# Kernel optimization log

Measured on AMD Instinct MI355X. Metric: run time of the kernel, lower is better.

The kernel has to match this reference:

```python
import jax, jax.numpy as jnp
import numpy as np

B, T, C, HS = 8, 2048, 1024, 128

def setup_inputs() -> dict:
    key = jax.random.key(0)
    kx, kq, kk, kv = jax.random.split(key, 4)
    x = jax.random.normal(kx, (B, T, C), dtype=jnp.float32)
    # torch Linear(C, HS, bias=False): y = x @ W^T with W [HS, C].
    # We store the transposed form [C, HS] and right-multiply (same math).
    scale = 1.0 / np.sqrt(C)  # torch default init scale-ish; exact init irrelevant for correctness
    Wq = jax.random.normal(kq, (C, HS), dtype=jnp.float32) * scale
    Wk = jax.random.normal(kk, (C, HS), dtype=jnp.float32) * scale
    Wv = jax.random.normal(kv, (C, HS), dtype=jnp.float32) * scale
    return {"x": x, "Wq": Wq, "Wk": Wk, "Wv": Wv}

def reference(x, Wq, Wk, Wv):
    Bx, Tx, Cx = x.shape
    q = x @ Wq  # [B, T, HS]
    k = x @ Wk
    v = x @ Wv
    # NOTE: original scales by C**-0.5 where C = n_embd (not head_size)
    wei = jnp.einsum('btd,bsd->bts', q, k) * (Cx ** -0.5)  # [B, T, T]
    causal = jnp.tril(jnp.ones((Tx, Tx), dtype=bool))
    wei = jnp.where(causal, wei, -jnp.inf)
    wei = jax.nn.softmax(wei, axis=-1)
    # dropout rate 0.0 (eval semantics) -> identity
    return jnp.einsum('bts,bsd->btd', wei, v)  # [B, T, HS]
```

## Files before the change

kernel.cpp:

```cpp
#include <hip/hip_runtime.h>
#include <hip/hip_bf16.h>
#include <stdint.h>

typedef float f32x4 __attribute__((ext_vector_type(4)));
typedef float f32x4v __attribute__((ext_vector_type(4)));
typedef short short8 __attribute__((ext_vector_type(8)));
typedef unsigned short u16;
typedef unsigned short u16x8 __attribute__((ext_vector_type(8)));
typedef unsigned short u16x4 __attribute__((ext_vector_type(4)));

#define MFMA16x16x32 __builtin_amdgcn_mfma_f32_16x16x32_bf16

__device__ __forceinline__ u16 f2bf(float f) {
    unsigned int u = __builtin_bit_cast(unsigned int, f);
    u += 0x7fffu + ((u >> 16) & 1u);
    return (u16)(u >> 16);
}

__device__ __forceinline__ void gload_lds16(const void* g, void* l) {
    __builtin_amdgcn_global_load_lds(
        (const __attribute__((address_space(1))) uint32_t*)g,
        (__attribute__((address_space(3))) uint32_t*)l, 16, 0, 0);
}

__device__ __forceinline__ int z_small(int na) {
    int za = (8 * na + 32) / 33;
    return za < 1 ? 1 : za;
}

__global__ void k_transpose_wf(const float* __restrict__ Wq, const float* __restrict__ Wk,
                               const float* __restrict__ Wv, u16* __restrict__ WTf) {
    int tid  = blockIdx.x * 256 + threadIdx.x;
    int f    = tid >> 6;
    int lane = tid & 63;
    int kt  = f / 48;
    int rem = f % 48;
    int ks  = rem / 24;
    int nc  = rem % 24;
    int col = nc * 16 + (lane & 15);
    int w   = col >> 7, n = col & 127;
    int k0  = kt * 64 + ks * 32 + (lane >> 4) * 8;
    const float* W = (w == 0) ? Wq : ((w == 1) ? Wk : Wv);
    u16x8 v;
#pragma unroll
    for (int j = 0; j < 8; ++j)
        v[j] = f2bf(W[(size_t)(k0 + j) * 128 + n]);
    *(u16x8*)(&WTf[(size_t)tid * 8]) = v;
}

__global__ __launch_bounds__(512) void k_qkv_gemm9(
    const float* __restrict__ x, const u16* __restrict__ WTf,
    u16* __restrict__ qb, u16* __restrict__ kb, u16* __restrict__ vT)
{
    __shared__ u16 abuf[2][64 * 64];
    __shared__ u16 bbuf[2][192 * 64];
    const int tid  = threadIdx.x;
    const int lane = tid & 63, wid = tid >> 6;
    const int wr = wid >> 2, wc = wid & 3;
    const int lrow = lane & 15, lk = lane >> 4;
    const int nh = blockIdx.x & 1;
    const int m0 = (blockIdx.x >> 1) * 64;

    const int arow = tid >> 3;
    const int aseg = tid & 7;
    const float* xsrc = x + (size_t)(m0 + arow) * 1024 + aseg * 8;

    f32x4 acc[2][3];
#pragma unroll
    for (int i = 0; i < 2; ++i)
#pragma unroll
        for (int j = 0; j < 3; ++j) acc[i][j] = (f32x4){0.f, 0.f, 0.f, 0.f};

#define LOADA(s0, s1, ktv)                                                     \
    s0 = *(const f32x4v*)(xsrc + (ktv) * 64);                                  \
    s1 = *(const f32x4v*)(xsrc + (ktv) * 64 + 4);

#define STOREA(buf, s0, s1)                                                    \
    {   u16x8 v;                                                               \
        v[0]=f2bf(s0[0]); v[1]=f2bf(s0[1]); v[2]=f2bf(s0[2]); v[3]=f2bf(s0[3]); \
        v[4]=f2bf(s1[0]); v[5]=f2bf(s1[1]); v[6]=f2bf(s1[2]); v[7]=f2bf(s1[3]); \
        *(u16x8*)(&buf[arow * 64 + ((aseg ^ (arow & 7)) << 3)]) = v; }

#define ISSUEB(buf, ktv)                                                       \
    {   const u16* bsrc = WTf + ((size_t)(ktv) * 48 + nh * 12) * 512;          \
        _Pragma("unroll") for (int i = 0; i < 3; ++i) {                        \
            int c   = tid + i * 512;                                           \
            int ks_ = c >> 9;                    \
            int r_  = c & 511;                                                 \
                    \
            ks_ = c / 768; r_ = c - ks_ * 768;                                 \
            gload_lds16(bsrc + ((size_t)ks_ * 24 + (r_ >> 6)) * 512 + (r_ & 63) * 8, \
                        &buf[c * 8]);                                          \
        } }

#define COMPUTE(ab, bb)                                                        \
    _Pragma("unroll") for (int ks = 0; ks < 2; ++ks) {                         \
        short8 af[2];                                                          \
        _Pragma("unroll") for (int mf = 0; mf < 2; ++mf) {                     \
            int row = wr * 32 + mf * 16 + lrow;                                \
            int blk = (ks * 4 + lk) ^ (row & 7);                               \
            af[mf] = *(const short8*)(&ab[row * 64 + (blk << 3)]);             \
        }                                                                      \
        _Pragma("unroll") for (int nf = 0; nf < 3; ++nf) {                     \
            short8 bfr = *(const short8*)(&bb[(ks * 12 + wc * 3 + nf) * 512 + lane * 8]); \
            _Pragma("unroll") for (int mf = 0; mf < 2; ++mf)                   \
                acc[mf][nf] = MFMA16x16x32(af[mf], bfr, acc[mf][nf], 0, 0, 0); \
        } }

#define WAITBAR()                                                              \
    asm volatile("s_waitcnt vmcnt(2) lgkmcnt(0)\n\ts_barrier" ::: "memory");   \
    __builtin_amdgcn_sched_barrier(0);

    f32x4v a0A, a1A, a0B, a1B;
    LOADA(a0A, a1A, 0);
    LOADA(a0B, a1B, 1);
    STOREA(abuf[0], a0A, a1A);
    ISSUEB(bbuf[0], 0);
    LOADA(a0A, a1A, 2);
    WAITBAR();

    for (int kt = 0; kt < 16; kt += 2) {
        {
            const int ktn = (kt + 1 < 16) ? kt + 1 : 15;
            ISSUEB(bbuf[1], ktn);
            __builtin_amdgcn_sched_barrier(0);
            COMPUTE(abuf[0], bbuf[0]);
            STOREA(abuf[1], a0B, a1B);
            const int kp = (kt + 3 < 16) ? kt + 3 : 15;
            LOADA(a0B, a1B, kp);
            WAITBAR();
        }
        {
            const int ktn = (kt + 2 < 16) ? kt + 2 : 15;
            ISSUEB(bbuf[0], ktn);
            __builtin_amdgcn_sched_barrier(0);
            COMPUTE(abuf[1], bbuf[1]);
            STOREA(abuf[0], a0A, a1A);
            const int kp = (kt + 4 < 16) ? kt + 4 : 15;
            LOADA(a0A, a1A, kp);
            WAITBAR();
        }
    }
#undef LOADA
#undef STOREA
#undef ISSUEB
#undef COMPUTE
#undef WAITBAR

#pragma unroll
    for (int nf = 0; nf < 3; ++nf) {
        const int gc   = nh * 192 + wc * 48 + nf * 16 + lrow;
        const int wsel = gc >> 7;
        const int col  = gc & 127;
#pragma unroll
        for (int mf = 0; mf < 2; ++mf) {
            const int row0 = m0 + wr * 32 + mf * 16 + lk * 4;
            if (wsel == 0) {
#pragma unroll
                for (int jj = 0; jj < 4; ++jj)
                    qb[(size_t)(row0 + jj) * 128 + col] = f2bf(acc[mf][nf][jj]);
            } else if (wsel == 1) {
#pragma unroll
                for (int jj = 0; jj < 4; ++jj)
                    kb[(size_t)(row0 + jj) * 128 + col] = f2bf(acc[mf][nf][jj]);
            } else {
                const int bb = row0 >> 11, t0 = row0 & 2047;
                u16x4 v;
#pragma unroll
                for (int jj = 0; jj < 4; ++jj) v[jj] = f2bf(acc[mf][nf][jj]);
                *(u16x4*)(&vT[((size_t)bb * 128 + col) * 2048 + t0]) = v;
            }
        }
    }
}

__global__ __launch_bounds__(256) void k_flash6(
    const u16* __restrict__ qb, const u16* __restrict__ kb, const u16* __restrict__ vT,
    float* __restrict__ po, float* __restrict__ pm, float* __restrict__ pl)
{
    __shared__ u16 k_lds[64 * 128];
    __shared__ u16 v_lds[128 * 64];
    __shared__ u16 p_lds[4 * 16 * 64];
    const int tid  = threadIdx.x;
    const int lane = tid & 63, wid = tid >> 6;
    const int lrow = lane & 15, lk = lane >> 4;
    const int bx = blockIdx.x;
    const int b  = bx & 7;
    const int p  = (bx >> 3) & 15;
    const int z  = bx >> 7;

    const int na = p + 1;
    const int za = z_small(na);
    int qt, n, k, Z;
    if (z < za) { qt = p;      n = na;     k = z;      Z = za;     }
    else        { qt = 31 - p; n = 32 - p; k = z - za; Z = 8 - za; }
    const int t0 = (k * n) / Z;
    const int t1 = ((k + 1) * n) / Z;

    const int qrow0 = qt * 64;
    short8 qf[4];
    {
        const u16* qp = qb + ((size_t)b * 2048 + qrow0 + wid * 16 + lrow) * 128;
#pragma unroll
        for (int ks = 0; ks < 4; ++ks) qf[ks] = *(const short8*)(qp + ks * 32 + lk * 8);
    }
    f32x4 of[8];
#pragma unroll
    for (int i = 0; i < 8; ++i) of[i] = (f32x4){0.f, 0.f, 0.f, 0.f};
    float mrun[4], lsum[4];
#pragma unroll
    for (int j = 0; j < 4; ++j) { mrun[j] = -1e30f; lsum[j] = 0.f; }

    const u16* kbase = kb + (size_t)b * 2048 * 128;
    const u16* vbase = vT + (size_t)b * 128 * 2048;
    u16* pw = p_lds + wid * (16 * 64);

    for (int t = t0; t < t1; ++t) {
        const int kv0 = t << 6;
        __syncthreads();
#pragma unroll
        for (int i = 0; i < 4; ++i) {
            int c = tid + i * 256;
            int row = c >> 4, blk = c & 15;
            gload_lds16(kbase + (size_t)(kv0 + row) * 128 + ((blk ^ (row & 7)) << 3),
                        &k_lds[c * 8]);
        }
#pragma unroll
        for (int i = 0; i < 4; ++i) {
            int c = tid + i * 256;
            int row = c >> 3, blk = c & 7;
            gload_lds16(vbase + (size_t)row * 2048 + kv0 + ((blk ^ (row & 7)) << 3),
                        &v_lds[c * 8]);
        }
        __syncthreads();

        f32x4 sf[4];
#pragma unroll
        for (int nf = 0; nf < 4; ++nf) sf[nf] = (f32x4){0.f, 0.f, 0.f, 0.f};
#pragma unroll
        for (int ks = 0; ks < 4; ++ks)
#pragma unroll
            for (int nf = 0; nf < 4; ++nf) {
                int row = nf * 16 + lrow;
                int blk = (ks * 4 + lk) ^ (row & 7);
                short8 bfr = *(const short8*)(&k_lds[row * 128 + (blk << 3)]);
                sf[nf] = MFMA16x16x32(qf[ks], bfr, sf[nf], 0, 0, 0);
            }

        const bool diag = (t == n - 1);
#pragma unroll
        for (int nf = 0; nf < 4; ++nf)
#pragma unroll
            for (int jj = 0; jj < 4; ++jj) {
                float s = sf[nf][jj] * 0.03125f;
                if (diag && (nf * 16 + lrow > wid * 16 + lk * 4 + jj)) s = -1e30f;
                sf[nf][jj] = s;
            }
        float mt[4];
#pragma unroll
        for (int jj = 0; jj < 4; ++jj)
            mt[jj] = fmaxf(fmaxf(sf[0][jj], sf[1][jj]), fmaxf(sf[2][jj], sf[3][jj]));
#pragma unroll
        for (int off = 1; off < 16; off <<= 1)
#pragma unroll
            for (int jj = 0; jj < 4; ++jj)
                mt[jj] = fmaxf(mt[jj], __shfl_xor(mt[jj], off));
        bool small = true;
#pragma unroll
        for (int jj = 0; jj < 4; ++jj) small = small && (mt[jj] <= mrun[jj] + 8.f);
        if (!__all(small)) {
#pragma unroll
            for (int jj = 0; jj < 4; ++jj) {
                float mnew = fmaxf(mrun[jj], mt[jj]);
                float sc   = __expf(mrun[jj] - mnew);
                mrun[jj]   = mnew;
                lsum[jj]  *= sc;
#pragma unroll
                for (int df = 0; df < 8; ++df) of[df][jj] *= sc;
            }
        }
        float rs[4] = {0.f, 0.f, 0.f, 0.f};
#pragma unroll
        for (int nf = 0; nf < 4; ++nf)
#pragma unroll
            for (int jj = 0; jj < 4; ++jj) {
                float e = __expf(sf[nf][jj] - mrun[jj]);
                sf[nf][jj] = e;
                rs[jj] += e;
            }
#pragma unroll
        for (int off = 1; off < 16; off <<= 1)
#pragma unroll
            for (int jj = 0; jj < 4; ++jj)
                rs[jj] += __shfl_xor(rs[jj], off);
#pragma unroll
        for (int jj = 0; jj < 4; ++jj) lsum[jj] += rs[jj];

#pragma unroll
        for (int nf = 0; nf < 4; ++nf)
#pragma unroll
            for (int jj = 0; jj < 4; ++jj) {
                int row = lk * 4 + jj;
                int col = nf * 16 + lrow;
                pw[row * 64 + (((col >> 3) ^ (row & 7)) << 3) + (col & 7)] = f2bf(sf[nf][jj]);
            }
        asm volatile("s_waitcnt lgkmcnt(0)" ::: "memory");
        __builtin_amdgcn_sched_barrier(0);
        short8 paf[2];
#pragma unroll
        for (int ks2 = 0; ks2 < 2; ++ks2) {
            int blk = (ks2 * 4 + lk) ^ (lrow & 7);
            paf[ks2] = *(const short8*)(&pw[lrow * 64 + (blk << 3)]);
        }
#pragma unroll
        for (int ks2 = 0; ks2 < 2; ++ks2)
#pragma unroll
            for (int df = 0; df < 8; ++df) {
                int row = df * 16 + lrow;
                int blk = (ks2 * 4 + lk) ^ (row & 7);
                short8 vf = *(const short8*)(&v_lds[row * 64 + (blk << 3)]);
                of[df] = MFMA16x16x32(paf[ks2], vf, of[df], 0, 0, 0);
            }
    }

    float* poslab = po + (size_t)bx * (64 * 128);
#pragma unroll
    for (int df = 0; df < 8; ++df)
#pragma unroll
        for (int jj = 0; jj < 4; ++jj)
            poslab[(size_t)(wid * 16 + lk * 4 + jj) * 128 + df * 16 + lrow] = of[df][jj];
    if (lrow == 0) {
#pragma unroll
        for (int jj = 0; jj < 4; ++jj) {
            pm[(size_t)bx * 64 + wid * 16 + lk * 4 + jj] = mrun[jj];
            pl[(size_t)bx * 64 + wid * 16 + lk * 4 + jj] = lsum[jj];
        }
    }
}

__global__ __launch_bounds__(256) void k_combine(
    const float* __restrict__ po, const float* __restrict__ pm, const float* __restrict__ pl,
    float* __restrict__ out)
{
    const int row  = blockIdx.x * 4 + (threadIdx.x >> 6);
    const int lane = threadIdx.x & 63;
    const int b  = row >> 11;
    const int t  = row & 2047;
    const int qt = t >> 6;
    const int r  = t & 63;

    const int p  = (qt < 16) ? qt : 31 - qt;
    const int za = z_small(p + 1);
    const int zlo = (qt < 16) ? 0 : za;
    const int zhi = (qt < 16) ? za : 8;

    float M = -1e30f;
    for (int z = zlo; z < zhi; ++z)
        M = fmaxf(M, pm[(size_t)(b + 8 * p + 128 * z) * 64 + r]);
    float den = 0.f, a0 = 0.f, a1 = 0.f;
    for (int z = zlo; z < zhi; ++z) {
        const int bxp = b + 8 * p + 128 * z;
        const float w = __expf(pm[(size_t)bxp * 64 + r] - M);
        den += w * pl[(size_t)bxp * 64 + r];
        const float* slab = po + ((size_t)bxp * 64 + r) * 128;
        a0 += w * slab[lane];
        a1 += w * slab[lane + 64];
    }
    const float inv = 1.f / den;
    out[(size_t)row * 128 + lane]      = a0 * inv;
    out[(size_t)row * 128 + lane + 64] = a1 * inv;
}

extern "C" void kernel_launch(void* const* d_in, const int* in_sizes, int n_in,
                              void* d_out, int out_size, void* d_ws, size_t ws_size,
                              hipStream_t stream) {
    const float* x  = (const float*)d_in[0];
    const float* Wq = (const float*)d_in[1];
    const float* Wk = (const float*)d_in[2];
    const float* Wv = (const float*)d_in[3];
    float* out = (float*)d_out;

    char* ws = (char*)d_ws;
    u16*   qb  = (u16*)(ws);
    u16*   kb  = (u16*)(ws + (size_t)4  * 1048576);
    u16*   vT  = (u16*)(ws + (size_t)8  * 1048576);
    u16*   WTf = (u16*)(ws + (size_t)12 * 1048576);
    float* po  = (float*)(ws + (size_t)13 * 1048576);
    float* pm  = (float*)(ws + (size_t)47 * 1048576);
    float* pl  = (float*)(ws + (size_t)48 * 1048576);

    k_transpose_wf<<<192, 256, 0, stream>>>(Wq, Wk, Wv, WTf);
    k_qkv_gemm9<<<512, 512, 0, stream>>>(x, WTf, qb, kb, vT);
    k_flash6<<<1024, 256, 0, stream>>>(qb, kb, vT, po, pm, pl);
    k_combine<<<4096, 256, 0, stream>>>(po, pm, pl, out);
}
```

Baseline: 81.67 us.

## Restructure QKV GEMM to single-buffered K=128 tiles with unrolled pipeline

The QKV projection GEMM drops double-buffered 64-wide K tiles and uses single LDS buffers holding 128-wide K tiles, so there are 8 iterations instead of 16, fully unrolled. The next B tile's async loads are issued only after a barrier that follows the compute, while x loads stay register-prefetched two steps ahead. This halves the number of barriers and loop iterations, but B loads now no longer overlap with compute, and each thread holds more prefetch registers.

```diff
diff --git a/kernel.cpp b/kernel.cpp
--- a/kernel.cpp
+++ b/kernel.cpp
@@ -48,12 +48,12 @@
     *(u16x8*)(&WTf[(size_t)tid * 8]) = v;
 }
 
-__global__ __launch_bounds__(512) void k_qkv_gemm9(
+__global__ __launch_bounds__(512) void k_qkv_gemm10(
     const float* __restrict__ x, const u16* __restrict__ WTf,
     u16* __restrict__ qb, u16* __restrict__ kb, u16* __restrict__ vT)
 {
-    __shared__ u16 abuf[2][64 * 64];
-    __shared__ u16 bbuf[2][192 * 64];
+    __shared__ u16 la[64 * 128];
+    __shared__ u16 bb[4 * 12 * 512];
     const int tid  = threadIdx.x;
     const int lane = tid & 63, wid = tid >> 6;
     const int wr = wid >> 2, wc = wid & 3;
@@ -63,7 +63,7 @@
 
     const int arow = tid >> 3;
     const int aseg = tid & 7;
-    const float* xsrc = x + (size_t)(m0 + arow) * 1024 + aseg * 8;
+    const float* xsrc = x + (size_t)(m0 + arow) * 1024 + aseg * 16;
 
     f32x4 acc[2][3];
 #pragma unroll
@@ -71,35 +71,39 @@
 #pragma unroll
         for (int j = 0; j < 3; ++j) acc[i][j] = (f32x4){0.f, 0.f, 0.f, 0.f};
 
-#define LOADA(s0, s1, ktv)                                                     \
-    s0 = *(const f32x4v*)(xsrc + (ktv) * 64);                                  \
-    s1 = *(const f32x4v*)(xsrc + (ktv) * 64 + 4);
-
-#define STOREA(buf, s0, s1)                                                    \
-    {   u16x8 v;                                                               \
-        v[0]=f2bf(s0[0]); v[1]=f2bf(s0[1]); v[2]=f2bf(s0[2]); v[3]=f2bf(s0[3]); \
-        v[4]=f2bf(s1[0]); v[5]=f2bf(s1[1]); v[6]=f2bf(s1[2]); v[7]=f2bf(s1[3]); \
-        *(u16x8*)(&buf[arow * 64 + ((aseg ^ (arow & 7)) << 3)]) = v; }
-
-#define ISSUEB(buf, ktv)                                                       \
-    {   const u16* bsrc = WTf + ((size_t)(ktv) * 48 + nh * 12) * 512;          \
-        _Pragma("unroll") for (int i = 0; i < 3; ++i) {                        \
-            int c   = tid + i * 512;                                           \
-            int ks_ = c >> 9;                    \
-            int r_  = c & 511;                                                 \
-                    \
-            ks_ = c / 768; r_ = c - ks_ * 768;                                 \
-            gload_lds16(bsrc + ((size_t)ks_ * 24 + (r_ >> 6)) * 512 + (r_ & 63) * 8, \
-                        &buf[c * 8]);                                          \
-        } }
-
-#define COMPUTE(ab, bb)                                                        \
-    _Pragma("unroll") for (int ks = 0; ks < 2; ++ks) {                         \
+#define LOADA(p0, p1, p2, p3, ktv)                                             \
+    p0 = *(const f32x4v*)(xsrc + (ktv) * 128);                                 \
+    p1 = *(const f32x4v*)(xsrc + (ktv) * 128 + 4);                             \
+    p2 = *(const f32x4v*)(xsrc + (ktv) * 128 + 8);                             \
+    p3 = *(const f32x4v*)(xsrc + (ktv) * 128 + 12);
+
+#define STOREA(p0, p1, p2, p3)                                                 \
+    {   u16x8 v0, v1;                                                          \
+        v0[0]=f2bf(p0[0]); v0[1]=f2bf(p0[1]); v0[2]=f2bf(p0[2]); v0[3]=f2bf(p0[3]); \
+        v0[4]=f2bf(p1[0]); v0[5]=f2bf(p1[1]); v0[6]=f2bf(p1[2]); v0[7]=f2bf(p1[3]); \
+        v1[0]=f2bf(p2[0]); v1[1]=f2bf(p2[1]); v1[2]=f2bf(p2[2]); v1[3]=f2bf(p2[3]); \
+        v1[4]=f2bf(p3[0]); v1[5]=f2bf(p3[1]); v1[6]=f2bf(p3[2]); v1[7]=f2bf(p3[3]); \
+        *(u16x8*)(&la[arow * 128 + (((2*aseg)   ^ (arow & 7)) << 3)]) = v0;     \
+        *(u16x8*)(&la[arow * 128 + (((2*aseg+1) ^ (arow & 7)) << 3)]) = v1; }
+
+#define ISSUEB(ktv)                                                            \
+    {   _Pragma("unroll") for (int i = 0; i < 6; ++i) {                        \
+            int c   = tid + i * 512;                   \
+            int ks_ = c / 768;                                                 \
+            int r_  = c - ks_ * 768;                     \
+            const u16* src = WTf + ((size_t)((ktv) * 4 + ks_) * 24 + nh * 12   \
+                                    + (r_ >> 6)) * 512 + (r_ & 63) * 8;        \
+            gload_lds16(src, &bb[c * 8]);                                      \
+        }                                                                      \
+        __builtin_amdgcn_sched_barrier(0); }
+
+#define COMPUTE()                                                              \
+    _Pragma("unroll") for (int ks = 0; ks < 4; ++ks) {                         \
         short8 af[2];                                                          \
         _Pragma("unroll") for (int mf = 0; mf < 2; ++mf) {                     \
             int row = wr * 32 + mf * 16 + lrow;                                \
             int blk = (ks * 4 + lk) ^ (row & 7);                               \
-            af[mf] = *(const short8*)(&ab[row * 64 + (blk << 3)]);             \
+            af[mf] = *(const short8*)(&la[row * 128 + (blk << 3)]);            \
         }                                                                      \
         _Pragma("unroll") for (int nf = 0; nf < 3; ++nf) {                     \
             short8 bfr = *(const short8*)(&bb[(ks * 12 + wc * 3 + nf) * 512 + lane * 8]); \
@@ -107,45 +111,52 @@
                 acc[mf][nf] = MFMA16x16x32(af[mf], bfr, acc[mf][nf], 0, 0, 0); \
         } }
 
-#define WAITBAR()                                                              \
-    asm volatile("s_waitcnt vmcnt(2) lgkmcnt(0)\n\ts_barrier" ::: "memory");   \
+#define BAR1()                                                                 \
+    asm volatile("s_waitcnt lgkmcnt(0)\n\ts_barrier" ::: "memory");            \
     __builtin_amdgcn_sched_barrier(0);
 
-    f32x4v a0A, a1A, a0B, a1B;
-    LOADA(a0A, a1A, 0);
-    LOADA(a0B, a1B, 1);
-    STOREA(abuf[0], a0A, a1A);
-    ISSUEB(bbuf[0], 0);
-    LOADA(a0A, a1A, 2);
-    WAITBAR();
-
-    for (int kt = 0; kt < 16; kt += 2) {
-        {
-            const int ktn = (kt + 1 < 16) ? kt + 1 : 15;
-            ISSUEB(bbuf[1], ktn);
-            __builtin_amdgcn_sched_barrier(0);
-            COMPUTE(abuf[0], bbuf[0]);
-            STOREA(abuf[1], a0B, a1B);
-            const int kp = (kt + 3 < 16) ? kt + 3 : 15;
-            LOADA(a0B, a1B, kp);
-            WAITBAR();
-        }
-        {
-            const int ktn = (kt + 2 < 16) ? kt + 2 : 15;
-            ISSUEB(bbuf[0], ktn);
-            __builtin_amdgcn_sched_barrier(0);
-            COMPUTE(abuf[1], bbuf[1]);
-            STOREA(abuf[0], a0A, a1A);
-            const int kp = (kt + 4 < 16) ? kt + 4 : 15;
-            LOADA(a0A, a1A, kp);
-            WAITBAR();
-        }
-    }
+#define WAITBAR4()                                                             \
+    asm volatile("s_waitcnt vmcnt(4) lgkmcnt(0)\n\ts_barrier" ::: "memory");   \
+    __builtin_amdgcn_sched_barrier(0);
+
+#define WAITBAR0()                                                             \
+    asm volatile("s_waitcnt vmcnt(0) lgkmcnt(0)\n\ts_barrier" ::: "memory");   \
+    __builtin_amdgcn_sched_barrier(0);
+
+    f32x4v a00, a01, a02, a03, a10, a11, a12, a13;
+    LOADA(a00, a01, a02, a03, 0);
+    LOADA(a10, a11, a12, a13, 1);
+    STOREA(a00, a01, a02, a03);
+    ISSUEB(0);
+    LOADA(a00, a01, a02, a03, 2);
+    WAITBAR4();
+
+    COMPUTE(); BAR1(); ISSUEB(1); STOREA(a10, a11, a12, a13);
+    LOADA(a10, a11, a12, a13, 3); WAITBAR4();
+    COMPUTE(); BAR1(); ISSUEB(2); STOREA(a00, a01, a02, a03);
+    LOADA(a00, a01, a02, a03, 4); WAITBAR4();
+    COMPUTE(); BAR1(); ISSUEB(3); STOREA(a10, a11, a12, a13);
+    LOADA(a10, a11, a12, a13, 5); WAITBAR4();
+    COMPUTE(); BAR1(); ISSUEB(4); STOREA(a00, a01, a02, a03);
+    LOADA(a00, a01, a02, a03, 6); WAITBAR4();
+    COMPUTE(); BAR1(); ISSUEB(5); STOREA(a10, a11, a12, a13);
+    LOADA(a10, a11, a12, a13, 7); WAITBAR4();
+    COMPUTE(); BAR1(); ISSUEB(6); STOREA(a00, a01, a02, a03);
+    WAITBAR0();
+    COMPUTE(); BAR1(); ISSUEB(7); STOREA(a10, a11, a12, a13);
+    WAITBAR0();
+    COMPUTE();
+
+    asm volatile("" :: "v"(a00[0]), "v"(a01[0]), "v"(a02[0]), "v"(a03[0]),
+                       "v"(a10[0]), "v"(a11[0]), "v"(a12[0]), "v"(a13[0]));
+
 #undef LOADA
 #undef STOREA
 #undef ISSUEB
 #undef COMPUTE
-#undef WAITBAR
+#undef BAR1
+#undef WAITBAR4
+#undef WAITBAR0
 
 #pragma unroll
     for (int nf = 0; nf < 3; ++nf) {
@@ -164,11 +175,11 @@
                 for (int jj = 0; jj < 4; ++jj)
                     kb[(size_t)(row0 + jj) * 128 + col] = f2bf(acc[mf][nf][jj]);
             } else {
-                const int bb = row0 >> 11, t0 = row0 & 2047;
+                const int bb2 = row0 >> 11, t0 = row0 & 2047;
                 u16x4 v;
 #pragma unroll
                 for (int jj = 0; jj < 4; ++jj) v[jj] = f2bf(acc[mf][nf][jj]);
-                *(u16x4*)(&vT[((size_t)bb * 128 + col) * 2048 + t0]) = v;
+                *(u16x4*)(&vT[((size_t)bb2 * 128 + col) * 2048 + t0]) = v;
             }
         }
     }
@@ -390,7 +401,7 @@
     float* pl  = (float*)(ws + (size_t)48 * 1048576);
 
     k_transpose_wf<<<192, 256, 0, stream>>>(Wq, Wk, Wv, WTf);
-    k_qkv_gemm9<<<512, 512, 0, stream>>>(x, WTf, qb, kb, vT);
+    k_qkv_gemm10<<<512, 512, 0, stream>>>(x, WTf, qb, kb, vT);
     k_flash6<<<1024, 256, 0, stream>>>(qb, kb, vT, po, pm, pl);
     k_combine<<<4096, 256, 0, stream>>>(po, pm, pl, out);
 }
```

Measured after the change: 85.17 us. 1.04x slower.
